# Kernel optimization log

Hardware: AMD Instinct MI355X
Metric: run time of the kernel (lower is better)

Reference implementation:

```python
import jax, jax.numpy as jnp
import numpy as np

B, N, H_DIM, G_DIM, G_HID, K_CONST = 32, 8192, 256, 256, 512, 64


def setup_inputs() -> dict:
    key = jax.random.key(0)
    k1, k2, k3 = jax.random.split(key, 3)
    hs = jax.random.normal(k1, (B, N, H_DIM), dtype=jnp.float32)
    # Sorted cluster labels 0..K-1, same row for all batch entries (training mode).
    cs_row = ((jnp.arange(N) * K_CONST) // N).astype(jnp.int32)
    cs_o = jnp.tile(cs_row[None, :], (B, 1))
    W1 = jax.random.normal(k2, (H_DIM, G_HID), dtype=jnp.float32) * (1.0 / np.sqrt(H_DIM))
    b1 = jnp.zeros((G_HID,), dtype=jnp.float32)
    W2 = jax.random.normal(k3, (G_HID, G_DIM), dtype=jnp.float32) * (1.0 / np.sqrt(G_HID))
    b2 = jnp.zeros((G_DIM,), dtype=jnp.float32)
    return {"hs": hs, "cs_o": cs_o, "W1": W1, "b1": b1, "W2": W2, "b2": b2,
            "n": N - 1, "K": K_CONST}


def reference(hs, cs_o, W1, b1, W2, b2, n, K):
    # Training mode (cs_is_sample=False): mask points >= n, use row 0 pattern.
    cs = cs_o.at[:, n:].set(-1)
    cs1 = cs[0]  # [N]
    # One-hot cluster membership: [K, N]
    onehot = (cs1[None, :] == jnp.arange(K)[:, None]).astype(hs.dtype)
    # Per-cluster sums H_k: [B, K, h_dim] (single pass, replaces K masked sweeps)
    Hk = jnp.einsum('kn,bnh->bkh', onehot, hs)
    hn = hs[:, n, :]  # [B, h_dim]
    # H = [H_0..H_{K-1}, H_0+h_n..H_{K-1}+h_n, h_n] -> [B, 2K+1, h_dim]
    H = jnp.concatenate([Hk, Hk + hn[:, None, :], hn[:, None, :]], axis=1)
    # g: 2-layer MLP applied rowwise
    gs = jax.nn.relu(H @ W1 + b1) @ W2 + b2  # [B, 2K+1, g_dim]
    # Exclude-sum combine: G[:,k] = sum_{j<K} gs[:,j] - gs[:,k] + gs[:,k+K]
    S = gs[:, :K, :].sum(axis=1)  # [B, g_dim]
    G_front = S[:, None, :] - gs[:, :K, :] + gs[:, K:2 * K, :]
    G_last = (S + gs[:, 2 * K, :])[:, None, :]
    G = jnp.concatenate([G_front, G_last], axis=1)  # [B, K+1, g_dim]
    G_mask = jnp.ones((hs.shape[0], K + 1), dtype=hs.dtype)
    return G, G_mask
```

## Files before the change

kernel.cpp:

```cpp
#include <hip/hip_runtime.h>

#define B_SZ   32
#define N_SZ   8192
#define HDIM   256
#define GHID   512
#define K_CL   64
#define M_ROWS (B_SZ * (2 * K_CL + 1))
#define M_PAD  4224

typedef short v8s __attribute__((ext_vector_type(8)));
typedef float v4f __attribute__((ext_vector_type(4)));

__device__ __forceinline__ unsigned short f32_to_bf16(float f) {
  unsigned int u = __float_as_uint(f);
  u += 0x7FFFu + ((u >> 16) & 1u);
  return (unsigned short)(u >> 16);
}

__device__ __forceinline__ int lower_bound_i(const int* __restrict__ a, int n, int key) {
  int lo = 0, hi = n;
  while (lo < hi) {
    const int mid = (lo + hi) >> 1;
    if (a[mid] < key) lo = mid + 1; else hi = mid;
  }
  return lo;
}

__global__ __launch_bounds__(256) void cluster_sum_kernel(
    const float* __restrict__ hs, const int* __restrict__ cs,
    const int* __restrict__ n_ptr, float* __restrict__ Hk) {
  const int b = blockIdx.x;
  const int k = blockIdx.y;
  const int tid = threadIdx.x;
  const int col = (tid & 63) * 4;
  const int rsub = tid >> 6;
  const int n_val = n_ptr[0];

  const int start = lower_bound_i(cs, N_SZ, k);
  int end = lower_bound_i(cs, N_SZ, k + 1);
  if (end > n_val) end = n_val;

  const float* base = hs + (size_t)b * N_SZ * HDIM + col;

  float4 a0 = make_float4(0.f, 0.f, 0.f, 0.f), a1 = a0, a2 = a0, a3 = a0;
  int r = start + rsub;
  for (; r + 12 < end; r += 16) {
    const float4 v0 = *(const float4*)(base + (size_t)(r) * HDIM);
    const float4 v1 = *(const float4*)(base + (size_t)(r + 4) * HDIM);
    const float4 v2 = *(const float4*)(base + (size_t)(r + 8) * HDIM);
    const float4 v3 = *(const float4*)(base + (size_t)(r + 12) * HDIM);
    a0.x += v0.x; a0.y += v0.y; a0.z += v0.z; a0.w += v0.w;
    a1.x += v1.x; a1.y += v1.y; a1.z += v1.z; a1.w += v1.w;
    a2.x += v2.x; a2.y += v2.y; a2.z += v2.z; a2.w += v2.w;
    a3.x += v3.x; a3.y += v3.y; a3.z += v3.z; a3.w += v3.w;
  }
  for (; r < end; r += 4) {
    const float4 v = *(const float4*)(base + (size_t)r * HDIM);
    a0.x += v.x; a0.y += v.y; a0.z += v.z; a0.w += v.w;
  }
  float4 acc;
  acc.x = (a0.x + a1.x) + (a2.x + a3.x);
  acc.y = (a0.y + a1.y) + (a2.y + a3.y);
  acc.z = (a0.z + a1.z) + (a2.z + a3.z);
  acc.w = (a0.w + a1.w) + (a2.w + a3.w);

  __shared__ float4 red[256];
  red[tid] = acc;
  __syncthreads();
  if (tid < 64) {
    const float4 p0 = red[tid], p1 = red[tid + 64], p2 = red[tid + 128], p3 = red[tid + 192];
    float4 o;
    o.x = (p0.x + p1.x) + (p2.x + p3.x);
    o.y = (p0.y + p1.y) + (p2.y + p3.y);
    o.z = (p0.z + p1.z) + (p2.z + p3.z);
    o.w = (p0.w + p1.w) + (p2.w + p3.w);
    *(float4*)(Hk + ((size_t)b * K_CL + k) * HDIM + tid * 4) = o;
  }
}

__global__ __launch_bounds__(256) void prep_kernel(
    const float* __restrict__ hs, const float* __restrict__ Hk,
    const float* __restrict__ W1, const float* __restrict__ W2,
    const int* __restrict__ n_ptr,
    unsigned short* __restrict__ Hbf, unsigned short* __restrict__ W1t,
    unsigned short* __restrict__ W2t) {
  const int idx = blockIdx.x;
  const int tid = threadIdx.x;

  if (idx < M_ROWS) {
    const int b = idx / 129;
    const int j = idx - b * 129;
    const int n_val = n_ptr[0];
    const float hn = hs[((size_t)b * N_SZ + n_val) * HDIM + tid];
    float v;
    if (j < K_CL)          v = Hk[((size_t)b * K_CL + j) * HDIM + tid];
    else if (j < 2 * K_CL) v = Hk[((size_t)b * K_CL + (j - K_CL)) * HDIM + tid] + hn;
    else                   v = hn;
    Hbf[(size_t)idx * HDIM + tid] = f32_to_bf16(v);
    return;
  }
  if (idx < M_PAD) {
    Hbf[(size_t)idx * HDIM + tid] = 0;
    return;
  }

  __shared__ float tile[32][33];
  if (idx < M_PAD + 128) {
    const int t = idx - M_PAD;
    const int tr = t >> 4, tc = t & 15;
    const int r0 = tid >> 5, c = tid & 31;
#pragma unroll
    for (int p = 0; p < 4; ++p) {
      const int r = p * 8 + r0;
      tile[r][c] = W1[(size_t)(tr * 32 + r) * GHID + tc * 32 + c];
    }
    __syncthreads();
#pragma unroll
    for (int p = 0; p < 4; ++p) {
      const int r = p * 8 + r0;
      W1t[(size_t)(tc * 32 + r) * HDIM + tr * 32 + c] = f32_to_bf16(tile[c][r]);
    }
  } else {
    const int t = idx - (M_PAD + 128);
    const int tr = t >> 3, tc = t & 7;
    const int r0 = tid >> 5, c = tid & 31;
#pragma unroll
    for (int p = 0; p < 4; ++p) {
      const int r = p * 8 + r0;
      tile[r][c] = W2[(size_t)(tr * 32 + r) * HDIM + tc * 32 + c];
    }
    __syncthreads();
#pragma unroll
    for (int p = 0; p < 4; ++p) {
      const int r = p * 8 + r0;
      W2t[(size_t)(tc * 32 + r) * GHID + tr * 32 + c] = f32_to_bf16(tile[c][r]);
    }
  }
}

template <int BN, int KDIM, bool RELU, bool OUT_BF16>
__global__ __launch_bounds__(256) void gemm_mfma_kernel(
    const unsigned short* __restrict__ A, const unsigned short* __restrict__ Bt,
    const float* __restrict__ bias, void* __restrict__ Cv, int N) {
  constexpr int BM = 128, BK = 32, LDT = 40;
  constexpr int CT = BN / 16;
  __shared__ unsigned short As[BM * LDT];
  __shared__ unsigned short Bs[BN * LDT];

  const int tid = threadIdx.x;
  const int wave = tid >> 6;
  const int lane = tid & 63;
  const int quad = lane >> 4;
  const int lr = lane & 15;
  const int row0 = blockIdx.x * BM;
  const int col0 = blockIdx.y * BN;

  const int sr = tid >> 2;
  const int sk = (tid & 3) * 8;

  v4f acc[2][CT];
#pragma unroll
  for (int rt = 0; rt < 2; ++rt)
#pragma unroll
    for (int ct = 0; ct < CT; ++ct) acc[rt][ct] = (v4f){0.f, 0.f, 0.f, 0.f};

  for (int k0 = 0; k0 < KDIM; k0 += BK) {
#pragma unroll
    for (int r = sr; r < BM; r += 64) {
      const uint4 v = *(const uint4*)(A + (size_t)(row0 + r) * KDIM + k0 + sk);
      *(uint4*)(As + r * LDT + sk) = v;
    }
#pragma unroll
    for (int r = sr; r < BN; r += 64) {
      const uint4 v = *(const uint4*)(Bt + (size_t)(col0 + r) * KDIM + k0 + sk);
      *(uint4*)(Bs + r * LDT + sk) = v;
    }
    __syncthreads();

    v8s a[2], bfr[CT];
#pragma unroll
    for (int rt = 0; rt < 2; ++rt)
      a[rt] = *(const v8s*)(As + (wave * 32 + rt * 16 + lr) * LDT + quad * 8);
#pragma unroll
    for (int ct = 0; ct < CT; ++ct)
      bfr[ct] = *(const v8s*)(Bs + (ct * 16 + lr) * LDT + quad * 8);

#pragma unroll
    for (int rt = 0; rt < 2; ++rt)
#pragma unroll
      for (int ct = 0; ct < CT; ++ct)
        acc[rt][ct] = __builtin_amdgcn_mfma_f32_16x16x32_bf16(
            a[rt], bfr[ct], acc[rt][ct], 0, 0, 0);
    __syncthreads();
  }

#pragma unroll
  for (int ct = 0; ct < CT; ++ct) {
    const int gcol = col0 + ct * 16 + lr;
    const float bv = bias[gcol];
#pragma unroll
    for (int rt = 0; rt < 2; ++rt) {
#pragma unroll
      for (int i = 0; i < 4; ++i) {
        const int grow = row0 + wave * 32 + rt * 16 + quad * 4 + i;
        float o = acc[rt][ct][i] + bv;
        if (RELU) o = fmaxf(o, 0.f);
        if (OUT_BF16)
          ((unsigned short*)Cv)[(size_t)grow * N + gcol] = f32_to_bf16(o);
        else
          ((float*)Cv)[(size_t)grow * N + gcol] = o;
      }
    }
  }
}

__global__ __launch_bounds__(64) void combine_kernel(
    const float* __restrict__ gs, float* __restrict__ G, float* __restrict__ mask) {
  const int b = blockIdx.x;
  const int h = blockIdx.y * 64 + threadIdx.x;
  const float* g = gs + (size_t)b * (2 * K_CL + 1) * HDIM + h;
  float S = 0.f;
#pragma unroll 8
  for (int k = 0; k < K_CL; ++k) S += g[k * HDIM];
#pragma unroll 4
  for (int k = 0; k < K_CL; ++k) {
    G[((size_t)b * (K_CL + 1) + k) * HDIM + h] = S - g[k * HDIM] + g[(K_CL + k) * HDIM];
  }
  G[((size_t)b * (K_CL + 1) + K_CL) * HDIM + h] = S + g[2 * K_CL * HDIM];
  const int mi = blockIdx.y * 64 + threadIdx.x;
  if (mi < K_CL + 1) mask[b * (K_CL + 1) + mi] = 1.0f;
}

extern "C" void kernel_launch(void* const* d_in, const int* in_sizes, int n_in,
                              void* d_out, int out_size, void* d_ws, size_t ws_size,
                              hipStream_t stream) {
  const float* hs = (const float*)d_in[0];
  const int* cs = (const int*)d_in[1];
  const float* W1 = (const float*)d_in[2];
  const float* b1 = (const float*)d_in[3];
  const float* W2 = (const float*)d_in[4];
  const float* b2 = (const float*)d_in[5];
  const int* n_ptr = (const int*)d_in[6];

  float* G = (float*)d_out;
  float* mask = G + (size_t)B_SZ * (K_CL + 1) * HDIM;

  char* w = (char*)d_ws;
  float* Hk = (float*)w;                 w += (size_t)B_SZ * K_CL * HDIM * 4;
  unsigned short* Hbf = (unsigned short*)w;  w += (size_t)M_PAD * HDIM * 2;
  unsigned short* W1t = (unsigned short*)w;  w += (size_t)GHID * HDIM * 2;
  unsigned short* W2t = (unsigned short*)w;  w += (size_t)HDIM * GHID * 2;
  unsigned short* act = (unsigned short*)w;  w += (size_t)M_PAD * GHID * 2;
  float* gs = (float*)w;

  cluster_sum_kernel<<<dim3(B_SZ, K_CL), 256, 0, stream>>>(hs, cs, n_ptr, Hk);
  prep_kernel<<<M_PAD + 256, 256, 0, stream>>>(hs, Hk, W1, W2, n_ptr, Hbf, W1t, W2t);
  gemm_mfma_kernel<128, HDIM, true, true><<<dim3(M_PAD / 128, GHID / 128), 256, 0, stream>>>(
      Hbf, W1t, b1, act, GHID);
  gemm_mfma_kernel<64, GHID, false, false><<<dim3(M_PAD / 128, HDIM / 64), 256, 0, stream>>>(
      act, W2t, b2, gs, HDIM);
  combine_kernel<<<dim3(B_SZ, HDIM / 64), 64, 0, stream>>>(gs, G, mask);
}
```

Measured before the change: 415.0 us.

## Fuse H-matrix construction into first GEMM and shrink GEMM row tiles

New measurement: 408.2 us. No clear change (-1.6%).

```diff
diff --git a/kernel.cpp b/kernel.cpp
--- a/kernel.cpp
+++ b/kernel.cpp
@@ -78,36 +78,15 @@
   }
 }
 
-__global__ __launch_bounds__(256) void prep_kernel(
-    const float* __restrict__ hs, const float* __restrict__ Hk,
+__global__ __launch_bounds__(256) void prep_w_kernel(
     const float* __restrict__ W1, const float* __restrict__ W2,
-    const int* __restrict__ n_ptr,
-    unsigned short* __restrict__ Hbf, unsigned short* __restrict__ W1t,
-    unsigned short* __restrict__ W2t) {
+    unsigned short* __restrict__ W1t, unsigned short* __restrict__ W2t) {
   const int idx = blockIdx.x;
   const int tid = threadIdx.x;
-
-  if (idx < M_ROWS) {
-    const int b = idx / 129;
-    const int j = idx - b * 129;
-    const int n_val = n_ptr[0];
-    const float hn = hs[((size_t)b * N_SZ + n_val) * HDIM + tid];
-    float v;
-    if (j < K_CL)          v = Hk[((size_t)b * K_CL + j) * HDIM + tid];
-    else if (j < 2 * K_CL) v = Hk[((size_t)b * K_CL + (j - K_CL)) * HDIM + tid] + hn;
-    else                   v = hn;
-    Hbf[(size_t)idx * HDIM + tid] = f32_to_bf16(v);
-    return;
-  }
-  if (idx < M_PAD) {
-    Hbf[(size_t)idx * HDIM + tid] = 0;
-    return;
-  }
-
   __shared__ float tile[32][33];
-  if (idx < M_PAD + 128) {
-    const int t = idx - M_PAD;
-    const int tr = t >> 4, tc = t & 15;
+
+  if (idx < 128) {
+    const int tr = idx >> 4, tc = idx & 15;
     const int r0 = tid >> 5, c = tid & 31;
 #pragma unroll
     for (int p = 0; p < 4; ++p) {
@@ -121,7 +100,7 @@
       W1t[(size_t)(tc * 32 + r) * HDIM + tr * 32 + c] = f32_to_bf16(tile[c][r]);
     }
   } else {
-    const int t = idx - (M_PAD + 128);
+    const int t = idx - 128;
     const int tr = t >> 3, tc = t & 7;
     const int r0 = tid >> 5, c = tid & 31;
 #pragma unroll
@@ -138,59 +117,69 @@
   }
 }
 
-template <int BN, int KDIM, bool RELU, bool OUT_BF16>
-__global__ __launch_bounds__(256) void gemm_mfma_kernel(
-    const unsigned short* __restrict__ A, const unsigned short* __restrict__ Bt,
-    const float* __restrict__ bias, void* __restrict__ Cv, int N) {
-  constexpr int BM = 128, BK = 32, LDT = 40;
+__global__ __launch_bounds__(256) void gemm1_kernel(
+    const float* __restrict__ hs, const float* __restrict__ Hk,
+    const unsigned short* __restrict__ W1t, const float* __restrict__ bias,
+    const int* __restrict__ n_ptr, unsigned short* __restrict__ act) {
+  constexpr int BM = 64, BN = 128, BK = 32, LDT = 40;
   constexpr int CT = BN / 16;
   __shared__ unsigned short As[BM * LDT];
   __shared__ unsigned short Bs[BN * LDT];
 
   const int tid = threadIdx.x;
-  const int wave = tid >> 6;
-  const int lane = tid & 63;
-  const int quad = lane >> 4;
-  const int lr = lane & 15;
+  const int wave = tid >> 6, lane = tid & 63;
+  const int quad = lane >> 4, lr = lane & 15;
   const int row0 = blockIdx.x * BM;
   const int col0 = blockIdx.y * BN;
+  const int n_val = n_ptr[0];
 
   const int sr = tid >> 2;
   const int sk = (tid & 3) * 8;
 
-  v4f acc[2][CT];
-#pragma unroll
-  for (int rt = 0; rt < 2; ++rt)
-#pragma unroll
-    for (int ct = 0; ct < CT; ++ct) acc[rt][ct] = (v4f){0.f, 0.f, 0.f, 0.f};
-
-  for (int k0 = 0; k0 < KDIM; k0 += BK) {
-#pragma unroll
-    for (int r = sr; r < BM; r += 64) {
-      const uint4 v = *(const uint4*)(A + (size_t)(row0 + r) * KDIM + k0 + sk);
-      *(uint4*)(As + r * LDT + sk) = v;
-    }
-#pragma unroll
-    for (int r = sr; r < BN; r += 64) {
-      const uint4 v = *(const uint4*)(Bt + (size_t)(col0 + r) * KDIM + k0 + sk);
-      *(uint4*)(Bs + r * LDT + sk) = v;
-    }
-    __syncthreads();
-
-    v8s a[2], bfr[CT];
-#pragma unroll
-    for (int rt = 0; rt < 2; ++rt)
-      a[rt] = *(const v8s*)(As + (wave * 32 + rt * 16 + lr) * LDT + quad * 8);
-#pragma unroll
-    for (int ct = 0; ct < CT; ++ct)
-      bfr[ct] = *(const v8s*)(Bs + (ct * 16 + lr) * LDT + quad * 8);
-
-#pragma unroll
-    for (int rt = 0; rt < 2; ++rt)
-#pragma unroll
-      for (int ct = 0; ct < CT; ++ct)
-        acc[rt][ct] = __builtin_amdgcn_mfma_f32_16x16x32_bf16(
-            a[rt], bfr[ct], acc[rt][ct], 0, 0, 0);
+  const int grow = row0 + sr;
+  const int b = grow / 129;
+  const int j = grow - b * 129;
+  const bool valid = (grow < M_ROWS);
+  const bool add_hn = valid && (j >= K_CL);
+  const bool use_hk = valid && (j < 2 * K_CL);
+  const int jj = (j < K_CL) ? j : (j - K_CL);
+  const float* hk_row = Hk + ((size_t)b * K_CL + jj) * HDIM + sk;
+  const float* hn_row = hs + ((size_t)b * N_SZ + n_val) * HDIM + sk;
+
+  v4f acc[CT];
+#pragma unroll
+  for (int ct = 0; ct < CT; ++ct) acc[ct] = (v4f){0.f, 0.f, 0.f, 0.f};
+
+  for (int k0 = 0; k0 < HDIM; k0 += BK) {
+    float4 f0 = make_float4(0.f, 0.f, 0.f, 0.f), f1 = f0;
+    if (use_hk) {
+      f0 = *(const float4*)(hk_row + k0);
+      f1 = *(const float4*)(hk_row + k0 + 4);
+    }
+    if (add_hn) {
+      const float4 h0 = *(const float4*)(hn_row + k0);
+      const float4 h1 = *(const float4*)(hn_row + k0 + 4);
+      f0.x += h0.x; f0.y += h0.y; f0.z += h0.z; f0.w += h0.w;
+      f1.x += h1.x; f1.y += h1.y; f1.z += h1.z; f1.w += h1.w;
+    }
+    unsigned short u[8];
+    u[0] = f32_to_bf16(f0.x); u[1] = f32_to_bf16(f0.y);
+    u[2] = f32_to_bf16(f0.z); u[3] = f32_to_bf16(f0.w);
+    u[4] = f32_to_bf16(f1.x); u[5] = f32_to_bf16(f1.y);
+    u[6] = f32_to_bf16(f1.z); u[7] = f32_to_bf16(f1.w);
+    *(uint4*)(As + sr * LDT + sk) = *(const uint4*)u;
+#pragma unroll
+    for (int r = sr; r < BN; r += 64)
+      *(uint4*)(Bs + r * LDT + sk) =
+          *(const uint4*)(W1t + (size_t)(col0 + r) * HDIM + k0 + sk);
+    __syncthreads();
+
+    const v8s a = *(const v8s*)(As + (wave * 16 + lr) * LDT + quad * 8);
+#pragma unroll
+    for (int ct = 0; ct < CT; ++ct) {
+      const v8s bf = *(const v8s*)(Bs + (ct * 16 + lr) * LDT + quad * 8);
+      acc[ct] = __builtin_amdgcn_mfma_f32_16x16x32_bf16(a, bf, acc[ct], 0, 0, 0);
+    }
     __syncthreads();
   }
 
@@ -199,17 +188,58 @@
     const int gcol = col0 + ct * 16 + lr;
     const float bv = bias[gcol];
 #pragma unroll
-    for (int rt = 0; rt < 2; ++rt) {
-#pragma unroll
-      for (int i = 0; i < 4; ++i) {
-        const int grow = row0 + wave * 32 + rt * 16 + quad * 4 + i;
-        float o = acc[rt][ct][i] + bv;
-        if (RELU) o = fmaxf(o, 0.f);
-        if (OUT_BF16)
-          ((unsigned short*)Cv)[(size_t)grow * N + gcol] = f32_to_bf16(o);
-        else
-          ((float*)Cv)[(size_t)grow * N + gcol] = o;
-      }
+    for (int i = 0; i < 4; ++i) {
+      const int orow = row0 + wave * 16 + quad * 4 + i;
+      act[(size_t)orow * GHID + gcol] = f32_to_bf16(fmaxf(acc[ct][i] + bv, 0.f));
+    }
+  }
+}
+
+__global__ __launch_bounds__(256) void gemm2_kernel(
+    const unsigned short* __restrict__ A, const unsigned short* __restrict__ Bt,
+    const float* __restrict__ bias, float* __restrict__ C) {
+  constexpr int BM = 64, BN = 64, BK = 32, LDT = 40;
+  constexpr int CT = BN / 16;
+  __shared__ unsigned short As[BM * LDT];
+  __shared__ unsigned short Bs[BN * LDT];
+
+  const int tid = threadIdx.x;
+  const int wave = tid >> 6, lane = tid & 63;
+  const int quad = lane >> 4, lr = lane & 15;
+  const int row0 = blockIdx.x * BM;
+  const int col0 = blockIdx.y * BN;
+
+  const int sr = tid >> 2;
+  const int sk = (tid & 3) * 8;
+
+  v4f acc[CT];
+#pragma unroll
+  for (int ct = 0; ct < CT; ++ct) acc[ct] = (v4f){0.f, 0.f, 0.f, 0.f};
+
+  for (int k0 = 0; k0 < GHID; k0 += BK) {
+    *(uint4*)(As + sr * LDT + sk) =
+        *(const uint4*)(A + (size_t)(row0 + sr) * GHID + k0 + sk);
+    *(uint4*)(Bs + sr * LDT + sk) =
+        *(const uint4*)(Bt + (size_t)(col0 + sr) * GHID + k0 + sk);
+    __syncthreads();
+
+    const v8s a = *(const v8s*)(As + (wave * 16 + lr) * LDT + quad * 8);
+#pragma unroll
+    for (int ct = 0; ct < CT; ++ct) {
+      const v8s bf = *(const v8s*)(Bs + (ct * 16 + lr) * LDT + quad * 8);
+      acc[ct] = __builtin_amdgcn_mfma_f32_16x16x32_bf16(a, bf, acc[ct], 0, 0, 0);
+    }
+    __syncthreads();
+  }
+
+#pragma unroll
+  for (int ct = 0; ct < CT; ++ct) {
+    const int gcol = col0 + ct * 16 + lr;
+    const float bv = bias[gcol];
+#pragma unroll
+    for (int i = 0; i < 4; ++i) {
+      const int orow = row0 + wave * 16 + quad * 4 + i;
+      C[(size_t)orow * HDIM + gcol] = acc[ct][i] + bv;
     }
   }
 }
@@ -246,18 +276,16 @@
   float* mask = G + (size_t)B_SZ * (K_CL + 1) * HDIM;
 
   char* w = (char*)d_ws;
-  float* Hk = (float*)w;                 w += (size_t)B_SZ * K_CL * HDIM * 4;
-  unsigned short* Hbf = (unsigned short*)w;  w += (size_t)M_PAD * HDIM * 2;
+  float* Hk = (float*)w;                     w += (size_t)B_SZ * K_CL * HDIM * 4;
   unsigned short* W1t = (unsigned short*)w;  w += (size_t)GHID * HDIM * 2;
   unsigned short* W2t = (unsigned short*)w;  w += (size_t)HDIM * GHID * 2;
   unsigned short* act = (unsigned short*)w;  w += (size_t)M_PAD * GHID * 2;
   float* gs = (float*)w;
 
   cluster_sum_kernel<<<dim3(B_SZ, K_CL), 256, 0, stream>>>(hs, cs, n_ptr, Hk);
-  prep_kernel<<<M_PAD + 256, 256, 0, stream>>>(hs, Hk, W1, W2, n_ptr, Hbf, W1t, W2t);
-  gemm_mfma_kernel<128, HDIM, true, true><<<dim3(M_PAD / 128, GHID / 128), 256, 0, stream>>>(
-      Hbf, W1t, b1, act, GHID);
-  gemm_mfma_kernel<64, GHID, false, false><<<dim3(M_PAD / 128, HDIM / 64), 256, 0, stream>>>(
-      act, W2t, b2, gs, HDIM);
+  prep_w_kernel<<<256, 256, 0, stream>>>(W1, W2, W1t, W2t);
+  gemm1_kernel<<<dim3(M_PAD / 64, GHID / 128), 256, 0, stream>>>(
+      hs, Hk, W1t, b1, n_ptr, act);
+  gemm2_kernel<<<dim3(M_PAD / 64, HDIM / 64), 256, 0, stream>>>(act, W2t, b2, gs);
   combine_kernel<<<dim3(B_SZ, HDIM / 64), 64, 0, stream>>>(gs, G, mask);
 }
```
